# Optimization experiments

Hardware: AMD Instinct MI355X
Metric: run time of the kernel (lower is better)

## Reference

```python
import jax, jax.numpy as jnp
import numpy as np

BRIGHTNESS_THRESHOLD = 0.4
NUM_BINS = 16


def _soft_histogram(x, mask):
    # x: [B, C, H, W], mask: [B, 1, H, W] (float 0/1)
    B, C, H, W = x.shape
    bin_centers = jnp.linspace(0.0, 1.0, NUM_BINS, dtype=x.dtype)  # [nb]
    bin_width = 1.0 / NUM_BINS
    inv_two_sigma2 = 1.0 / (2.0 * bin_width * bin_width)
    x_flat = x.reshape(B, C, H * W, 1)            # [B,C,HW,1]
    mask_flat = mask.reshape(B, 1, H * W, 1)      # [B,1,HW,1]
    weights = jnp.exp(-((x_flat - bin_centers) ** 2) * inv_two_sigma2)  # [B,C,HW,nb]
    hist = jnp.sum(weights * mask_flat, axis=2)   # [B,C,nb]
    hist = hist / (jnp.sum(hist, axis=-1, keepdims=True) + 1e-7)
    return hist


def setup_inputs() -> dict:
    key = jax.random.key(0)
    k1, k2 = jax.random.split(key)
    pred = jax.random.uniform(k1, (8, 3, 512, 512), dtype=jnp.float32)
    target = jax.random.uniform(k2, (8, 3, 512, 512), dtype=jnp.float32)
    return {"pred": pred, "target": target}


def reference(pred, target):
    target_brightness = jnp.mean(target, axis=1, keepdims=True)       # [B,1,H,W]
    bright_mask = (target_brightness > BRIGHTNESS_THRESHOLD).astype(pred.dtype)
    pred_hist = _soft_histogram(pred, bright_mask)
    target_hist = _soft_histogram(target, bright_mask)
    return jnp.mean(jnp.abs(pred_hist - target_hist))
```

## Files before the change

### kernel.cpp

```cpp
#include <hip/hip_runtime.h>

#define NB 16
#define BATCH 8
#define PLANE (512*512)
#define FBINS 512
#define CHUNKS 128
#define THREADS 256
#define PX_PER_BLOCK (PLANE / CHUNKS)
#define GROUPS (PX_PER_BLOCK / (THREADS * 4))
#define SLICES 8
#define FPB (FBINS / SLICES)

#if __has_builtin(__builtin_amdgcn_exp2f)
__device__ __forceinline__ float exp2_fast(float x) { return __builtin_amdgcn_exp2f(x); }
#else
__device__ __forceinline__ float exp2_fast(float x) { return __expf(x * 0.69314718056f); }
#endif

#define NEG_C2 (-0.8207331788f)

__device__ __forceinline__ int qbin(float x) {
    int f = (int)(x * (float)FBINS);
    return f > (FBINS - 1) ? (FBINS - 1) : f;
}

__global__ __launch_bounds__(THREADS)
void count_kernel(const float* __restrict__ pred,
                  const float* __restrict__ tgt,
                  unsigned int* __restrict__ partial
                  )
{
    const int chunk = blockIdx.x;
    const int b     = blockIdx.y;
    const int tid   = threadIdx.x;

    __shared__ unsigned int cnt[3 * FBINS];
    #pragma unroll
    for (int k = 0; k < 3 * FBINS / THREADS; ++k)
        cnt[tid + k * THREADS] = 0u;
    __syncthreads();

    const float* pb = pred + (size_t)b * 3 * PLANE;
    const float* tb = tgt  + (size_t)b * 3 * PLANE;
    const int base = chunk * PX_PER_BLOCK + tid * 4;

    #pragma unroll
    for (int g = 0; g < GROUPS; ++g) {
        const int p = base + g * (THREADS * 4);
        const float4 P0 = *(const float4*)(pb + p);
        const float4 P1 = *(const float4*)(pb + PLANE + p);
        const float4 P2 = *(const float4*)(pb + 2 * PLANE + p);
        const float4 T0 = *(const float4*)(tb + p);
        const float4 T1 = *(const float4*)(tb + PLANE + p);
        const float4 T2 = *(const float4*)(tb + 2 * PLANE + p);

        const float p0a[4] = {P0.x, P0.y, P0.z, P0.w};
        const float p1a[4] = {P1.x, P1.y, P1.z, P1.w};
        const float p2a[4] = {P2.x, P2.y, P2.z, P2.w};
        const float t0a[4] = {T0.x, T0.y, T0.z, T0.w};
        const float t1a[4] = {T1.x, T1.y, T1.z, T1.w};
        const float t2a[4] = {T2.x, T2.y, T2.z, T2.w};

        #pragma unroll
        for (int j = 0; j < 4; ++j) {
            const bool m = (t0a[j] + t1a[j] + t2a[j]) * (1.0f / 3.0f) > 0.4f;
            if (m) {
                atomicAdd(&cnt[           qbin(p0a[j])], 1u);
                atomicAdd(&cnt[           qbin(p1a[j])], 65536u);
                atomicAdd(&cnt[FBINS    + qbin(p2a[j])], 1u);
                atomicAdd(&cnt[FBINS    + qbin(t0a[j])], 65536u);
                atomicAdd(&cnt[2*FBINS  + qbin(t1a[j])], 1u);
                atomicAdd(&cnt[2*FBINS  + qbin(t2a[j])], 65536u);
            }
        }
    }
    __syncthreads();

    #pragma unroll
    for (int k = 0; k < 3 * FBINS / THREADS; ++k) {
        const int w  = tid + k * THREADS;
        const int h2 = w >> 9;
        const int f  = w & (FBINS - 1);
        partial[(((size_t)h2 * BATCH + b) * CHUNKS + chunk) * FBINS + f] = cnt[w];
    }
}

__global__ __launch_bounds__(THREADS)
void combine_kernel(const unsigned int* __restrict__ partial,
                    float* __restrict__ out2 )
{
    const int slice = blockIdx.x;
    const int hb    = blockIdx.y;
    const int h     = hb / BATCH;
    const int b     = hb % BATCH;
    const int h2    = h >> 1;
    const int sh    = (h & 1) * 16;
    const int tid   = threadIdx.x;

    const int f_loc = tid & (FPB - 1);
    const int q     = tid >> 6;
    const int f     = slice * FPB + f_loc;

    const unsigned int* base =
        partial + (((size_t)h2 * BATCH + b) * CHUNKS + q * 32) * FBINS + f;
    unsigned int s = 0u;
    #pragma unroll 8
    for (int c = 0; c < 32; ++c)
        s += (base[(size_t)c * FBINS] >> sh) & 0xFFFFu;

    __shared__ unsigned int red[4][FPB];
    red[q][f_loc] = s;
    __syncthreads();

    if (tid < FPB) {
        const float cf = (float)(red[0][tid] + red[1][tid] + red[2][tid] + red[3][tid]);
        const float y  = ((float)(slice * FPB + tid) + 0.5f) * (15.0f / (float)FBINS);

        float acc[NB];
        #pragma unroll
        for (int i = 0; i < NB; ++i) {
            const float u = y - (float)i;
            acc[i] = cf * exp2_fast(u * u * NEG_C2);
        }
        #pragma unroll
        for (int off = 32; off > 0; off >>= 1)
            #pragma unroll
            for (int i = 0; i < NB; ++i)
                acc[i] += __shfl_down(acc[i], off, 64);

        if (tid == 0) {
            float* o = out2 + ((size_t)slice * 48 + hb) * NB;
            #pragma unroll
            for (int i = 0; i < NB; ++i) o[i] = acc[i];
        }
    }
}

__global__ void finalize_kernel(const float* __restrict__ out2,
                                float* __restrict__ out)
{
    const int t = threadIdx.x;
    __shared__ float H[48 * NB];

    for (int e = t; e < 48 * NB; e += 384) {
        float v = 0.0f;
        #pragma unroll
        for (int s = 0; s < SLICES; ++s)
            v += out2[(size_t)s * 48 * NB + e];
        H[e] = v;
    }
    __syncthreads();

    const int b   = t / 48;
    const int rem = t % 48;
    const int c   = rem / NB;
    const int i   = rem % NB;

    const float* hp = H + ((c    ) * BATCH + b) * NB;
    const float* ht = H + ((c + 3) * BATCH + b) * NB;
    float sp = 0.0f, st = 0.0f;
    #pragma unroll
    for (int k = 0; k < NB; ++k) { sp += hp[k]; st += ht[k]; }

    float val = fabsf(hp[i] / (sp + 1e-7f) - ht[i] / (st + 1e-7f));

    #pragma unroll
    for (int off = 32; off > 0; off >>= 1)
        val += __shfl_down(val, off, 64);

    __shared__ float r[6];
    const int lane = t & 63, wv = t >> 6;
    if (lane == 0) r[wv] = val;
    __syncthreads();
    if (t == 0)
        out[0] = (r[0] + r[1] + r[2] + r[3] + r[4] + r[5]) * (1.0f / 384.0f);
}

extern "C" void kernel_launch(void* const* d_in, const int* in_sizes, int n_in,
                              void* d_out, int out_size, void* d_ws, size_t ws_size,
                              hipStream_t stream)
{
    const float* pred = (const float*)d_in[0];
    const float* tgt  = (const float*)d_in[1];

    unsigned int* partial = (unsigned int*)d_ws;
    float* out2 = (float*)((char*)d_ws + (size_t)3 * BATCH * CHUNKS * FBINS * 4);

    count_kernel<<<dim3(CHUNKS, BATCH), THREADS, 0, stream>>>(pred, tgt, partial);
    combine_kernel<<<dim3(SLICES, 48), THREADS, 0, stream>>>(partial, out2);
    finalize_kernel<<<1, 384, 0, stream>>>(out2, (float*)d_out);
}
```

Before: 90.89 us.

## Fuse Gaussian bin projection into count kernel and drop combine kernel

Each count block now builds a shared-memory table of Gaussian weights for every fine bin and projects its local 512-bin counts onto the 16 output bins. It writes 96 floats per block instead of 1536 packed counters. The separate combine kernel is removed, and finalize sums the per-chunk partials directly. This removes one launch and most of the partial-buffer traffic. In exchange, every block pays for computing the 32 KB table and the projection, and the larger shared-memory footprint may reduce occupancy.

After: 93.89 us. 3.3% more time.

```diff
diff --git a/kernel.cpp b/kernel.cpp
--- a/kernel.cpp
+++ b/kernel.cpp
@@ -8,8 +8,7 @@
 #define THREADS 256
 #define PX_PER_BLOCK (PLANE / CHUNKS)
 #define GROUPS (PX_PER_BLOCK / (THREADS * 4))
-#define SLICES 8
-#define FPB (FBINS / SLICES)
+#define NOUT 96
 
 #if __has_builtin(__builtin_amdgcn_exp2f)
 __device__ __forceinline__ float exp2_fast(float x) { return __builtin_amdgcn_exp2f(x); }
@@ -27,17 +26,29 @@
 __global__ __launch_bounds__(THREADS)
 void count_kernel(const float* __restrict__ pred,
                   const float* __restrict__ tgt,
-                  unsigned int* __restrict__ partial
-                  )
+                  float* __restrict__ partial )
 {
     const int chunk = blockIdx.x;
     const int b     = blockIdx.y;
     const int tid   = threadIdx.x;
 
     __shared__ unsigned int cnt[3 * FBINS];
+    __shared__ float wtab[FBINS * NB];
+    __shared__ float pout[2][NOUT];
+
     #pragma unroll
     for (int k = 0; k < 3 * FBINS / THREADS; ++k)
         cnt[tid + k * THREADS] = 0u;
+
+    #pragma unroll
+    for (int k = 0; k < FBINS * NB / THREADS; ++k) {
+        const int e = tid + k * THREADS;
+        const int f = e >> 4;
+        const int i = e & 15;
+        const float y = ((float)f + 0.5f) * (15.0f / (float)FBINS);
+        const float u = y - (float)i;
+        wtab[e] = exp2_fast(u * u * NEG_C2);
+    }
     __syncthreads();
 
     const float* pb = pred + (size_t)b * 3 * PLANE;
@@ -76,104 +87,78 @@
     }
     __syncthreads();
 
-    #pragma unroll
-    for (int k = 0; k < 3 * FBINS / THREADS; ++k) {
-        const int w  = tid + k * THREADS;
-        const int h2 = w >> 9;
-        const int f  = w & (FBINS - 1);
-        partial[(((size_t)h2 * BATCH + b) * CHUNKS + chunk) * FBINS + f] = cnt[w];
-    }
-}
+    if (tid < 2 * NOUT) {
+        const int o    = tid % NOUT;
+        const int half = tid / NOUT;
+        const int ch   = o >> 4;
+        const int i    = o & 15;
+        const int ch2  = ch >> 1;
+        const int sh   = (ch & 1) * 16;
 
-__global__ __launch_bounds__(THREADS)
-void combine_kernel(const unsigned int* __restrict__ partial,
-                    float* __restrict__ out2 )
-{
-    const int slice = blockIdx.x;
-    const int hb    = blockIdx.y;
-    const int h     = hb / BATCH;
-    const int b     = hb % BATCH;
-    const int h2    = h >> 1;
-    const int sh    = (h & 1) * 16;
-    const int tid   = threadIdx.x;
-
-    const int f_loc = tid & (FPB - 1);
-    const int q     = tid >> 6;
-    const int f     = slice * FPB + f_loc;
-
-    const unsigned int* base =
-        partial + (((size_t)h2 * BATCH + b) * CHUNKS + q * 32) * FBINS + f;
-    unsigned int s = 0u;
-    #pragma unroll 8
-    for (int c = 0; c < 32; ++c)
-        s += (base[(size_t)c * FBINS] >> sh) & 0xFFFFu;
-
-    __shared__ unsigned int red[4][FPB];
-    red[q][f_loc] = s;
-    __syncthreads();
-
-    if (tid < FPB) {
-        const float cf = (float)(red[0][tid] + red[1][tid] + red[2][tid] + red[3][tid]);
-        const float y  = ((float)(slice * FPB + tid) + 0.5f) * (15.0f / (float)FBINS);
-
-        float acc[NB];
-        #pragma unroll
-        for (int i = 0; i < NB; ++i) {
-            const float u = y - (float)i;
-            acc[i] = cf * exp2_fast(u * u * NEG_C2);
+        float acc = 0.0f;
+        const int f0 = half * (FBINS / 2);
+        #pragma unroll 8
+        for (int f = f0; f < f0 + FBINS / 2; ++f) {
+            const float cf = (float)((cnt[ch2 * FBINS + f] >> sh) & 0xFFFFu);
+            acc = fmaf(cf, wtab[(f << 4) + i], acc);
         }
-        #pragma unroll
-        for (int off = 32; off > 0; off >>= 1)
-            #pragma unroll
-            for (int i = 0; i < NB; ++i)
-                acc[i] += __shfl_down(acc[i], off, 64);
-
-        if (tid == 0) {
-            float* o = out2 + ((size_t)slice * 48 + hb) * NB;
-            #pragma unroll
-            for (int i = 0; i < NB; ++i) o[i] = acc[i];
-        }
-    }
-}
-
-__global__ void finalize_kernel(const float* __restrict__ out2,
-                                float* __restrict__ out)
-{
-    const int t = threadIdx.x;
-    __shared__ float H[48 * NB];
-
-    for (int e = t; e < 48 * NB; e += 384) {
-        float v = 0.0f;
-        #pragma unroll
-        for (int s = 0; s < SLICES; ++s)
-            v += out2[(size_t)s * 48 * NB + e];
-        H[e] = v;
+        pout[half][o] = acc;
     }
     __syncthreads();
 
-    const int b   = t / 48;
-    const int rem = t % 48;
-    const int c   = rem / NB;
-    const int i   = rem % NB;
+    if (tid < NOUT)
+        partial[((size_t)b * CHUNKS + chunk) * NOUT + tid] =
+            pout[0][tid] + pout[1][tid];
+}
 
-    const float* hp = H + ((c    ) * BATCH + b) * NB;
-    const float* ht = H + ((c + 3) * BATCH + b) * NB;
-    float sp = 0.0f, st = 0.0f;
-    #pragma unroll
-    for (int k = 0; k < NB; ++k) { sp += hp[k]; st += ht[k]; }
+__global__ __launch_bounds__(768)
+void finalize_kernel(const float* __restrict__ partial,
+                     float* __restrict__ out)
+{
+    const int t = threadIdx.x;
+    __shared__ float H[BATCH * NOUT];
 
-    float val = fabsf(hp[i] / (sp + 1e-7f) - ht[i] / (st + 1e-7f));
+    {
+        const int b = t / NOUT;
+        const int o = t % NOUT;
+        const float* base = partial + (size_t)b * CHUNKS * NOUT + o;
+        float v = 0.0f;
+        #pragma unroll 8
+        for (int c = 0; c < CHUNKS; ++c)
+            v += base[(size_t)c * NOUT];
+        H[t] = v;
+    }
+    __syncthreads();
+
+    float val = 0.0f;
+    if (t < 384) {
+        const int b   = t / 48;
+        const int rem = t % 48;
+        const int c   = rem / NB;
+        const int i   = rem % NB;
+
+        const float* hp = H + b * NOUT + (c    ) * NB;
+        const float* ht = H + b * NOUT + (c + 3) * NB;
+        float sp = 0.0f, st = 0.0f;
+        #pragma unroll
+        for (int k = 0; k < NB; ++k) { sp += hp[k]; st += ht[k]; }
+        val = fabsf(hp[i] / (sp + 1e-7f) - ht[i] / (st + 1e-7f));
+    }
 
     #pragma unroll
     for (int off = 32; off > 0; off >>= 1)
         val += __shfl_down(val, off, 64);
 
-    __shared__ float r[6];
+    __shared__ float r[12];
     const int lane = t & 63, wv = t >> 6;
     if (lane == 0) r[wv] = val;
     __syncthreads();
-    if (t == 0)
-        out[0] = (r[0] + r[1] + r[2] + r[3] + r[4] + r[5]) * (1.0f / 384.0f);
+    if (t == 0) {
+        float s = 0.0f;
+        #pragma unroll
+        for (int w = 0; w < 6; ++w) s += r[w];
+        out[0] = s * (1.0f / 384.0f);
+    }
 }
 
 extern "C" void kernel_launch(void* const* d_in, const int* in_sizes, int n_in,
@@ -183,10 +168,8 @@
     const float* pred = (const float*)d_in[0];
     const float* tgt  = (const float*)d_in[1];
 
-    unsigned int* partial = (unsigned int*)d_ws;
-    float* out2 = (float*)((char*)d_ws + (size_t)3 * BATCH * CHUNKS * FBINS * 4);
+    float* partial = (float*)d_ws;
 
     count_kernel<<<dim3(CHUNKS, BATCH), THREADS, 0, stream>>>(pred, tgt, partial);
-    combine_kernel<<<dim3(SLICES, 48), THREADS, 0, stream>>>(partial, out2);
-    finalize_kernel<<<1, 384, 0, stream>>>(out2, (float*)d_out);
+    finalize_kernel<<<1, 768, 0, stream>>>(partial, (float*)d_out);
 }
```
